# Optimization experiments

Hardware: AMD Instinct MI355X
Metric: run time of the kernel (lower is better)

Reference implementation:

```python
import jax, jax.numpy as jnp
import numpy as np

N_USER, N_BOOK, E = 150000, 75000, 1500000
D_USER, D_BOOK, H = 64, 128, 128
N_LAYERS = 3
EPS = 1e-5


def setup_inputs() -> dict:
    key = jax.random.key(0)
    ks = jax.random.split(key, 16)
    s = 1.0 / np.sqrt(H)
    inp = {
        "user_x": jax.random.normal(ks[0], (N_USER, D_USER), jnp.float32),
        "book_x": jax.random.normal(ks[1], (N_BOOK, D_BOOK), jnp.float32),
        "edge_src": jax.random.randint(ks[2], (E,), 0, N_USER, jnp.int32),
        "edge_dst": jax.random.randint(ks[3], (E,), 0, N_BOOK, jnp.int32),
        "user_proj_w": jax.random.normal(ks[4], (D_USER, H), jnp.float32) / np.sqrt(D_USER),
        "user_proj_b": jnp.zeros((H,), jnp.float32),
        "book_proj_w": jax.random.normal(ks[5], (D_BOOK, H), jnp.float32) / np.sqrt(D_BOOK),
        "book_proj_b": jnp.zeros((H,), jnp.float32),
        "Wl": jax.random.normal(ks[6], (N_LAYERS, H, H), jnp.float32) * s,
        "bl": jnp.zeros((N_LAYERS, H), jnp.float32),
        "Wr": jax.random.normal(ks[7], (N_LAYERS, H, H), jnp.float32) * s,
        "user_gamma": jnp.ones((H,), jnp.float32),
        "user_beta": jnp.zeros((H,), jnp.float32),
        "book_gamma": jnp.ones((H,), jnp.float32),
        "book_beta": jnp.zeros((H,), jnp.float32),
    }
    return inp


def _sage(x_src, x_dst, src_idx, dst_idx, n_dst, wl, bl, wr):
    # mean-aggregate neighbor messages, then lin_l(mean) + lin_r(x_dst)
    msg = x_src[src_idx]                                   # [E, H] gather
    summed = jax.ops.segment_sum(msg, dst_idx, num_segments=n_dst)
    cnt = jax.ops.segment_sum(jnp.ones((src_idx.shape[0],), x_src.dtype),
                              dst_idx, num_segments=n_dst)
    mean = summed / jnp.maximum(cnt, 1.0)[:, None]
    return mean @ wl + bl + x_dst @ wr


def _layernorm(x, gamma, beta):
    mu = jnp.mean(x, axis=-1, keepdims=True)
    var = jnp.mean(jnp.square(x - mu), axis=-1, keepdims=True)
    return (x - mu) * jax.lax.rsqrt(var + EPS) * gamma + beta


def reference(user_x, book_x, edge_src, edge_dst,
              user_proj_w, user_proj_b, book_proj_w, book_proj_b,
              Wl, bl, Wr, user_gamma, user_beta, book_gamma, book_beta):
    u = user_x @ user_proj_w + user_proj_b   # [N_user, H]
    b = book_x @ book_proj_w + book_proj_b   # [N_book, H]
    for i in range(Wl.shape[0]):
        # shared SAGEConv weights for both directions (same module instance)
        new_b = _sage(u, b, edge_src, edge_dst, b.shape[0], Wl[i], bl[i], Wr[i])
        new_u = _sage(b, u, edge_dst, edge_src, u.shape[0], Wl[i], bl[i], Wr[i])
        u = jax.nn.relu(new_u)
        b = jax.nn.relu(new_b)
        # dropout is identity in eval mode
    u = _layernorm(u, user_gamma, user_beta)
    b = _layernorm(b, book_gamma, book_beta)
    return u, b
```

## Files before the change

kernel.cpp:

```cpp
#include <hip/hip_runtime.h>

#define NU 150000
#define NB 75000
#define NE 1500000
#define DU 64
#define DB 128
#define HD 128
#define NL 3

#define UBLK ((NU + 255) / 256)
#define BBLK ((NB + 255) / 256)

typedef unsigned short ushort_t;
typedef unsigned int uint_t;
using short8 = __attribute__((ext_vector_type(8))) short;
using f32x4  = __attribute__((ext_vector_type(4))) float;

__device__ inline ushort_t f2bf(float f) {
    uint_t x = __builtin_bit_cast(uint_t, f);
    x += 0x7fffu + ((x >> 16) & 1u);
    return (ushort_t)(x >> 16);
}
__device__ inline float bf_lo(uint_t v) { return __builtin_bit_cast(float, v << 16); }
__device__ inline float bf_hi(uint_t v) { return __builtin_bit_cast(float, v & 0xffff0000u); }

__global__ void hist_kernel(const int* __restrict__ src, const int* __restrict__ dst,
                            int* __restrict__ deg_u, int* __restrict__ deg_b, int n) {
    int e = blockIdx.x * blockDim.x + threadIdx.x;
    if (e >= n) return;
    atomicAdd(&deg_u[src[e]], 1);
    atomicAdd(&deg_b[dst[e]], 1);
}

__global__ __launch_bounds__(256) void assign_kernel(
        const int* __restrict__ deg_u, const int* __restrict__ deg_b,
        int* __restrict__ ptr_u, int* __restrict__ cur_u,
        int* __restrict__ ptr_b, int* __restrict__ cur_b,
        int* __restrict__ counters) {
    __shared__ int wave_tot[4];
    __shared__ int block_base;
    int blk = blockIdx.x;
    int t = threadIdx.x;
    int lane = t & 63, wid = t >> 6;

    const int* deg; int* ptr; int* cur; int idx; int valid_n; int* counter;
    if (blk < UBLK) {
        deg = deg_u; ptr = ptr_u; cur = cur_u; counter = counters;
        idx = blk * 256 + t; valid_n = NU;
    } else {
        deg = deg_b; ptr = ptr_b; cur = cur_b; counter = counters + 1;
        idx = (blk - UBLK) * 256 + t; valid_n = NB;
    }
    int d = (idx < valid_n) ? deg[idx] : 0;

    int v = d;
#pragma unroll
    for (int s = 1; s < 64; s <<= 1) {
        int nv = __shfl_up(v, s);
        if (lane >= s) v += nv;
    }
    if (lane == 63) wave_tot[wid] = v;
    __syncthreads();
    if (t == 0) {
        int run = 0;
#pragma unroll
        for (int w = 0; w < 4; ++w) { int c = wave_tot[w]; wave_tot[w] = run; run += c; }
        block_base = atomicAdd(counter, run);
    }
    __syncthreads();
    if (idx < valid_n) {
        int start = block_base + wave_tot[wid] + v - d;
        ptr[idx] = start;
        cur[idx] = start;
    }
}

__global__ void fill_kernel(const int* __restrict__ src, const int* __restrict__ dst,
                            int* __restrict__ cur_u, int* __restrict__ cur_b,
                            int* __restrict__ adj_u, int* __restrict__ adj_b, int n) {
    int e = blockIdx.x * blockDim.x + threadIdx.x;
    if (e >= n) return;
    int s = src[e], d = dst[e];
    adj_b[atomicAdd(&cur_b[d], 1)] = s;
    adj_u[atomicAdd(&cur_u[s], 1)] = d;
}

__global__ __launch_bounds__(256) void prep_weights(
        const float* __restrict__ upw, const float* __restrict__ bpw,
        const float* __restrict__ Wl, const float* __restrict__ Wr,
        ushort_t* __restrict__ upwt, ushort_t* __restrict__ bpwt,
        ushort_t* __restrict__ Wlt, ushort_t* __restrict__ Wrt) {
    int m = blockIdx.x;
    const float* src; ushort_t* dst; int K;
    if (m == 0)      { src = upw; dst = upwt; K = DU; }
    else if (m == 1) { src = bpw; dst = bpwt; K = HD; }
    else if (m < 5)  { src = Wl + (m - 2) * HD * HD; dst = Wlt + (m - 2) * HD * HD; K = HD; }
    else             { src = Wr + (m - 5) * HD * HD; dst = Wrt + (m - 5) * HD * HD; K = HD; }
    for (int i = threadIdx.x; i < K * HD; i += blockDim.x) {
        int k = i >> 7, n = i & 127;
        dst[n * K + k] = f2bf(src[i]);
    }
}

__global__ __launch_bounds__(256) void aggregate_bf16(
        const ushort_t* __restrict__ xsrc, const int* __restrict__ adj,
        const int* __restrict__ ptr, const int* __restrict__ deg,
        ushort_t* __restrict__ out, int n) {
    int wave = (blockIdx.x * blockDim.x + threadIdx.x) >> 6;
    int lane = threadIdx.x & 63;
    if (wave >= n) return;
    int start = ptr[wave];
    int d = deg[wave];
    int end = start + d;
    const uint_t* s4 = (const uint_t*)xsrc;
    float ax = 0.f, ay = 0.f;
    int j = start;
    for (; j + 4 <= end; j += 4) {
        int i0 = adj[j], i1 = adj[j + 1], i2 = adj[j + 2], i3 = adj[j + 3];
        uint_t v0 = s4[(size_t)i0 * 64 + lane];
        uint_t v1 = s4[(size_t)i1 * 64 + lane];
        uint_t v2 = s4[(size_t)i2 * 64 + lane];
        uint_t v3 = s4[(size_t)i3 * 64 + lane];
        ax += bf_lo(v0) + bf_lo(v1) + bf_lo(v2) + bf_lo(v3);
        ay += bf_hi(v0) + bf_hi(v1) + bf_hi(v2) + bf_hi(v3);
    }
    for (; j < end; ++j) {
        uint_t v = s4[(size_t)adj[j] * 64 + lane];
        ax += bf_lo(v); ay += bf_hi(v);
    }
    float inv = 1.0f / (float)(d > 0 ? d : 1);
    uint_t packed = (uint_t)f2bf(ax * inv) | ((uint_t)f2bf(ay * inv) << 16);
    ((uint_t*)out)[(size_t)wave * 64 + lane] = packed;
}


template <bool FP32>
__device__ inline void stage_A(const void* __restrict__ src, int row0, int N, int K,
                               int k0, ushort_t* __restrict__ lds, int tid) {
    int c = (tid & 3) * 8;
    int r = tid >> 2;
#pragma unroll
    for (int h = 0; h < 2; ++h) {
        int rr = r + h * 64;
        int grow = row0 + rr;
        if constexpr (FP32) {
            ushort_t tmp[8];
            if (grow < N) {
                const float* p = (const float*)src + (size_t)grow * K + k0 + c;
                float4 v0 = *(const float4*)p;
                float4 v1 = *(const float4*)(p + 4);
                tmp[0] = f2bf(v0.x); tmp[1] = f2bf(v0.y); tmp[2] = f2bf(v0.z); tmp[3] = f2bf(v0.w);
                tmp[4] = f2bf(v1.x); tmp[5] = f2bf(v1.y); tmp[6] = f2bf(v1.z); tmp[7] = f2bf(v1.w);
            } else {
#pragma unroll
                for (int q = 0; q < 8; ++q) tmp[q] = 0;
            }
            *(short8*)&lds[rr * 40 + c] = *(const short8*)tmp;
        } else {
            short8 v = {};
            if (grow < N)
                v = *(const short8*)((const ushort_t*)src + (size_t)grow * K + k0 + c);
            *(short8*)&lds[rr * 40 + c] = v;
        }
    }
}

__device__ inline void stage_W(const ushort_t* __restrict__ Wt, int K, int k0,
                               ushort_t* __restrict__ lds, int tid) {
    int c = (tid & 3) * 8;
    int r = tid >> 2;
#pragma unroll
    for (int h = 0; h < 2; ++h) {
        int rr = r + h * 64;
        *(short8*)&lds[rr * 40 + c] = *(const short8*)(Wt + (size_t)rr * K + k0 + c);
    }
}

__device__ inline void mm_step(const ushort_t* __restrict__ a_lds,
                               const ushort_t* __restrict__ w_lds,
                               f32x4 acc[2][8], int wv, int l) {
    int lr = l & 15, lg = l >> 4;
    short8 af0 = *(const short8*)&a_lds[(wv * 32 + lr) * 40 + lg * 8];
    short8 af1 = *(const short8*)&a_lds[(wv * 32 + 16 + lr) * 40 + lg * 8];
#pragma unroll
    for (int nf = 0; nf < 8; ++nf) {
        short8 bfv = *(const short8*)&w_lds[(nf * 16 + lr) * 40 + lg * 8];
        acc[0][nf] = __builtin_amdgcn_mfma_f32_16x16x32_bf16(af0, bfv, acc[0][nf], 0, 0, 0);
        acc[1][nf] = __builtin_amdgcn_mfma_f32_16x16x32_bf16(af1, bfv, acc[1][nf], 0, 0, 0);
    }
}

template <int K1, bool A_FP32, bool HAS_X, bool DO_RELU, bool DO_LN>
__global__ __launch_bounds__(256) void gemm_bf16(
        const void* __restrict__ A, const ushort_t* __restrict__ X,
        const ushort_t* __restrict__ W1t, const ushort_t* __restrict__ W2t,
        const float* __restrict__ bias,
        const float* __restrict__ gamma, const float* __restrict__ beta,
        void* __restrict__ OUT, int N) {
    __shared__ ushort_t a_lds[128 * 40];
    __shared__ ushort_t w_lds[128 * 40];

    const int tid = threadIdx.x;
    const int l = tid & 63;
    const int wv = tid >> 6;
    const int row0 = blockIdx.x * 128;
    const int lr = l & 15, lg = l >> 4;

    f32x4 acc[2][8];
#pragma unroll
    for (int mf = 0; mf < 2; ++mf)
#pragma unroll
        for (int nf = 0; nf < 8; ++nf) acc[mf][nf] = (f32x4){0.f, 0.f, 0.f, 0.f};

#pragma unroll
    for (int k0 = 0; k0 < K1; k0 += 32) {
        __syncthreads();
        stage_A<A_FP32>(A, row0, N, K1, k0, a_lds, tid);
        stage_W(W1t, K1, k0, w_lds, tid);
        __syncthreads();
        mm_step(a_lds, w_lds, acc, wv, l);
    }
    if constexpr (HAS_X) {
#pragma unroll
        for (int k0 = 0; k0 < HD; k0 += 32) {
            __syncthreads();
            stage_A<false>(X, row0, N, HD, k0, a_lds, tid);
            stage_W(W2t, HD, k0, w_lds, tid);
            __syncthreads();
            mm_step(a_lds, w_lds, acc, wv, l);
        }
    }

    if constexpr (DO_LN) {
#pragma unroll
        for (int mf = 0; mf < 2; ++mf) {
#pragma unroll
            for (int j = 0; j < 4; ++j) {
                int grow = row0 + wv * 32 + mf * 16 + lg * 4 + j;
                float vals[8];
                float sum = 0.f, sq = 0.f;
#pragma unroll
                for (int nf = 0; nf < 8; ++nf) {
                    float v = acc[mf][nf][j] + bias[nf * 16 + lr];
                    v = fmaxf(v, 0.f);
                    vals[nf] = v; sum += v; sq += v * v;
                }
#pragma unroll
                for (int off = 8; off > 0; off >>= 1) {
                    sum += __shfl_xor(sum, off, 16);
                    sq  += __shfl_xor(sq,  off, 16);
                }
                float mu = sum * (1.0f / 128.0f);
                float var = sq * (1.0f / 128.0f) - mu * mu;
                float rs = rsqrtf(var + 1e-5f);
                if (grow < N) {
                    float* op = (float*)OUT + (size_t)grow * HD;
#pragma unroll
                    for (int nf = 0; nf < 8; ++nf) {
                        int col = nf * 16 + lr;
                        op[col] = (vals[nf] - mu) * rs * gamma[col] + beta[col];
                    }
                }
            }
        }
    } else {
#pragma unroll
        for (int mf = 0; mf < 2; ++mf) {
#pragma unroll
            for (int nf = 0; nf < 8; ++nf) {
                float bv = bias[nf * 16 + lr];
                int col = nf * 16 + lr;
#pragma unroll
                for (int j = 0; j < 4; ++j) {
                    int grow = row0 + wv * 32 + mf * 16 + lg * 4 + j;
                    float v = acc[mf][nf][j] + bv;
                    if constexpr (DO_RELU) v = fmaxf(v, 0.f);
                    if (grow < N)
                        ((ushort_t*)OUT)[(size_t)grow * HD + col] = f2bf(v);
                }
            }
        }
    }
}

extern "C" void kernel_launch(void* const* d_in, const int* in_sizes, int n_in,
                              void* d_out, int out_size, void* d_ws, size_t ws_size,
                              hipStream_t stream) {
    const float* user_x      = (const float*)d_in[0];
    const float* book_x      = (const float*)d_in[1];
    const int*   edge_src    = (const int*)d_in[2];
    const int*   edge_dst    = (const int*)d_in[3];
    const float* user_proj_w = (const float*)d_in[4];
    const float* user_proj_b = (const float*)d_in[5];
    const float* book_proj_w = (const float*)d_in[6];
    const float* book_proj_b = (const float*)d_in[7];
    const float* Wl          = (const float*)d_in[8];
    const float* blb         = (const float*)d_in[9];
    const float* Wr          = (const float*)d_in[10];
    const float* user_gamma  = (const float*)d_in[11];
    const float* user_beta   = (const float*)d_in[12];
    const float* book_gamma  = (const float*)d_in[13];
    const float* book_beta   = (const float*)d_in[14];

    char* ws = (char*)d_ws;
    size_t off = 0;
    auto alloc = [&](size_t bytes) { char* p = ws + off; off += (bytes + 255) & ~(size_t)255; return p; };
    ushort_t* u_s0 = (ushort_t*)alloc((size_t)NU * HD * 2);
    ushort_t* u_s1 = (ushort_t*)alloc((size_t)NU * HD * 2);
    ushort_t* b_s0 = (ushort_t*)alloc((size_t)NB * HD * 2);
    ushort_t* b_s1 = (ushort_t*)alloc((size_t)NB * HD * 2);
    int* adj_u = (int*)alloc((size_t)NE * 4);
    int* adj_b = (int*)alloc((size_t)NE * 4);
    int* deg_u = (int*)alloc((size_t)NU * 4);
    int* deg_b = (int*)alloc((size_t)NB * 4);
    int* ptr_u = (int*)alloc((size_t)NU * 4);
    int* ptr_b = (int*)alloc((size_t)NB * 4);
    int* cur_u = (int*)alloc((size_t)NU * 4);
    int* cur_b = (int*)alloc((size_t)NB * 4);
    int* counters = (int*)alloc(2 * 4);
    ushort_t* upwt = (ushort_t*)alloc((size_t)HD * DU * 2);
    ushort_t* bpwt = (ushort_t*)alloc((size_t)HD * HD * 2);
    ushort_t* Wlt  = (ushort_t*)alloc((size_t)NL * HD * HD * 2);
    ushort_t* Wrt  = (ushort_t*)alloc((size_t)NL * HD * HD * 2);
    (void)ws_size; (void)in_sizes; (void)n_in; (void)out_size;

    float* out_u = (float*)d_out;
    float* out_b = out_u + (size_t)NU * HD;

    hipMemsetAsync(deg_u, 0, (size_t)NU * 4, stream);
    hipMemsetAsync(deg_b, 0, (size_t)NB * 4, stream);
    hipMemsetAsync(counters, 0, 2 * 4, stream);
    hist_kernel<<<(NE + 255) / 256, 256, 0, stream>>>(edge_src, edge_dst, deg_u, deg_b, NE);
    assign_kernel<<<UBLK + BBLK, 256, 0, stream>>>(deg_u, deg_b, ptr_u, cur_u, ptr_b, cur_b, counters);
    fill_kernel<<<(NE + 255) / 256, 256, 0, stream>>>(edge_src, edge_dst, cur_u, cur_b, adj_u, adj_b, NE);

    prep_weights<<<8, 256, 0, stream>>>(user_proj_w, book_proj_w, Wl, Wr, upwt, bpwt, Wlt, Wrt);

    gemm_bf16<DU, true, false, false, false><<<(NU + 127) / 128, 256, 0, stream>>>(
        user_x, nullptr, upwt, nullptr, user_proj_b, nullptr, nullptr, u_s0, NU);
    gemm_bf16<DB, true, false, false, false><<<(NB + 127) / 128, 256, 0, stream>>>(
        book_x, nullptr, bpwt, nullptr, book_proj_b, nullptr, nullptr, b_s0, NB);

    ushort_t* u_cur = u_s0; ushort_t* u_alt = u_s1;
    ushort_t* b_cur = b_s0; ushort_t* b_alt = b_s1;

    for (int li = 0; li < NL; ++li) {
        const ushort_t* wlt = Wlt + (size_t)li * HD * HD;
        const ushort_t* wrt = Wrt + (size_t)li * HD * HD;
        const float* bb = blb + (size_t)li * HD;
        bool last = (li == NL - 1);

        aggregate_bf16<<<(NB + 3) / 4, 256, 0, stream>>>(u_cur, adj_b, ptr_b, deg_b, b_alt, NB);
        aggregate_bf16<<<(NU + 3) / 4, 256, 0, stream>>>(b_cur, adj_u, ptr_u, deg_u, u_alt, NU);

        if (!last) {
            gemm_bf16<HD, false, true, true, false><<<(NB + 127) / 128, 256, 0, stream>>>(
                b_alt, b_cur, wlt, wrt, bb, nullptr, nullptr, b_alt, NB);
            gemm_bf16<HD, false, true, true, false><<<(NU + 127) / 128, 256, 0, stream>>>(
                u_alt, u_cur, wlt, wrt, bb, nullptr, nullptr, u_alt, NU);
        } else {
            gemm_bf16<HD, false, true, false, true><<<(NB + 127) / 128, 256, 0, stream>>>(
                b_alt, b_cur, wlt, wrt, bb, book_gamma, book_beta, out_b, NB);
            gemm_bf16<HD, false, true, false, true><<<(NU + 127) / 128, 256, 0, stream>>>(
                u_alt, u_cur, wlt, wrt, bb, user_gamma, user_beta, out_u, NU);
        }

        ushort_t* t;
        t = u_cur; u_cur = u_alt; u_alt = t;
        t = b_cur; b_cur = b_alt; b_alt = t;
    }
}
```

Before: 1.232 ms.

## Partition CSR fill into node-range passes and widen aggregate gathers to 8 bytes

The CSR fill kernel is split into 8 launches. Each launch only writes adjacency entries for one slice of user and book ids, so the atomics and scattered writes hit a smaller, more cache-resident region of memory. The cost is reading the edge arrays 8 times. The aggregation kernel now has each half-wave process a different neighbor with 8-byte loads per lane, then combines the two halves with a cross-lane shuffle, so more neighbor rows are in flight per iteration.

Result: faster. 1.125 ms (-8.7%).

```diff
diff --git a/kernel.cpp b/kernel.cpp
--- a/kernel.cpp
+++ b/kernel.cpp
@@ -7,6 +7,7 @@
 #define DB 128
 #define HD 128
 #define NL 3
+#define FILLP 8
 
 #define UBLK ((NU + 255) / 256)
 #define BBLK ((NB + 255) / 256)
@@ -75,14 +76,15 @@
     }
 }
 
-__global__ void fill_kernel(const int* __restrict__ src, const int* __restrict__ dst,
+__global__ void fill_ranged(const int* __restrict__ src, const int* __restrict__ dst,
                             int* __restrict__ cur_u, int* __restrict__ cur_b,
-                            int* __restrict__ adj_u, int* __restrict__ adj_b, int n) {
+                            int* __restrict__ adj_u, int* __restrict__ adj_b, int n,
+                            int ulo, int uhi, int blo, int bhi) {
     int e = blockIdx.x * blockDim.x + threadIdx.x;
     if (e >= n) return;
     int s = src[e], d = dst[e];
-    adj_b[atomicAdd(&cur_b[d], 1)] = s;
-    adj_u[atomicAdd(&cur_u[s], 1)] = d;
+    if (s >= ulo && s < uhi) adj_u[atomicAdd(&cur_u[s], 1)] = d;
+    if (d >= blo && d < bhi) adj_b[atomicAdd(&cur_b[d], 1)] = s;
 }
 
 __global__ __launch_bounds__(256) void prep_weights(
@@ -112,25 +114,45 @@
     int start = ptr[wave];
     int d = deg[wave];
     int end = start + d;
-    const uint_t* s4 = (const uint_t*)xsrc;
-    float ax = 0.f, ay = 0.f;
+    int half = lane >> 5, sl = lane & 31;
+    const uint2* s8 = (const uint2*)xsrc;
+    float a0 = 0.f, a1 = 0.f, a2 = 0.f, a3 = 0.f;
     int j = start;
-    for (; j + 4 <= end; j += 4) {
-        int i0 = adj[j], i1 = adj[j + 1], i2 = adj[j + 2], i3 = adj[j + 3];
-        uint_t v0 = s4[(size_t)i0 * 64 + lane];
-        uint_t v1 = s4[(size_t)i1 * 64 + lane];
-        uint_t v2 = s4[(size_t)i2 * 64 + lane];
-        uint_t v3 = s4[(size_t)i3 * 64 + lane];
-        ax += bf_lo(v0) + bf_lo(v1) + bf_lo(v2) + bf_lo(v3);
-        ay += bf_hi(v0) + bf_hi(v1) + bf_hi(v2) + bf_hi(v3);
-    }
-    for (; j < end; ++j) {
-        uint_t v = s4[(size_t)adj[j] * 64 + lane];
-        ax += bf_lo(v); ay += bf_hi(v);
-    }
-    float inv = 1.0f / (float)(d > 0 ? d : 1);
-    uint_t packed = (uint_t)f2bf(ax * inv) | ((uint_t)f2bf(ay * inv) << 16);
-    ((uint_t*)out)[(size_t)wave * 64 + lane] = packed;
+    for (; j + 8 <= end; j += 8) {
+        int i0 = adj[j + half];
+        int i1 = adj[j + 2 + half];
+        int i2 = adj[j + 4 + half];
+        int i3 = adj[j + 6 + half];
+        uint2 v0 = s8[(size_t)i0 * 32 + sl];
+        uint2 v1 = s8[(size_t)i1 * 32 + sl];
+        uint2 v2 = s8[(size_t)i2 * 32 + sl];
+        uint2 v3 = s8[(size_t)i3 * 32 + sl];
+        a0 += bf_lo(v0.x) + bf_lo(v1.x) + bf_lo(v2.x) + bf_lo(v3.x);
+        a1 += bf_hi(v0.x) + bf_hi(v1.x) + bf_hi(v2.x) + bf_hi(v3.x);
+        a2 += bf_lo(v0.y) + bf_lo(v1.y) + bf_lo(v2.y) + bf_lo(v3.y);
+        a3 += bf_hi(v0.y) + bf_hi(v1.y) + bf_hi(v2.y) + bf_hi(v3.y);
+    }
+    for (; j + 2 <= end; j += 2) {
+        int i = adj[j + half];
+        uint2 v = s8[(size_t)i * 32 + sl];
+        a0 += bf_lo(v.x); a1 += bf_hi(v.x); a2 += bf_lo(v.y); a3 += bf_hi(v.y);
+    }
+    if (j < end && half == 0) {
+        int i = adj[j];
+        uint2 v = s8[(size_t)i * 32 + sl];
+        a0 += bf_lo(v.x); a1 += bf_hi(v.x); a2 += bf_lo(v.y); a3 += bf_hi(v.y);
+    }
+    a0 += __shfl_xor(a0, 32);
+    a1 += __shfl_xor(a1, 32);
+    a2 += __shfl_xor(a2, 32);
+    a3 += __shfl_xor(a3, 32);
+    if (half == 0) {
+        float inv = 1.0f / (float)(d > 0 ? d : 1);
+        uint2 o;
+        o.x = (uint_t)f2bf(a0 * inv) | ((uint_t)f2bf(a1 * inv) << 16);
+        o.y = (uint_t)f2bf(a2 * inv) | ((uint_t)f2bf(a3 * inv) << 16);
+        ((uint2*)out)[(size_t)wave * 32 + sl] = o;
+    }
 }
 
 
@@ -332,7 +354,12 @@
     hipMemsetAsync(counters, 0, 2 * 4, stream);
     hist_kernel<<<(NE + 255) / 256, 256, 0, stream>>>(edge_src, edge_dst, deg_u, deg_b, NE);
     assign_kernel<<<UBLK + BBLK, 256, 0, stream>>>(deg_u, deg_b, ptr_u, cur_u, ptr_b, cur_b, counters);
-    fill_kernel<<<(NE + 255) / 256, 256, 0, stream>>>(edge_src, edge_dst, cur_u, cur_b, adj_u, adj_b, NE);
+    for (int p = 0; p < FILLP; ++p) {
+        int ulo = (int)((size_t)NU * p / FILLP), uhi = (int)((size_t)NU * (p + 1) / FILLP);
+        int blo = (int)((size_t)NB * p / FILLP), bhi = (int)((size_t)NB * (p + 1) / FILLP);
+        fill_ranged<<<(NE + 255) / 256, 256, 0, stream>>>(
+            edge_src, edge_dst, cur_u, cur_b, adj_u, adj_b, NE, ulo, uhi, blo, bhi);
+    }
 
     prep_weights<<<8, 256, 0, stream>>>(user_proj_w, book_proj_w, Wl, Wr, upwt, bpwt, Wlt, Wrt);
 
```
